# Kernel tuning notes

Hardware: AMD Instinct MI355X
Metric: run time of the kernel (lower is better)

The kernel has to match this reference:

```python
import jax, jax.numpy as jnp
import numpy as np

EPS = 1e-5
P = 2  # polynomial kernel degree


def setup_inputs() -> dict:
    key = jax.random.key(0)
    k1, k2, k3 = jax.random.split(key, 3)
    b, t, h, d = 2, 2048, 8, 64
    Q = jax.random.normal(k1, (b, t, h, d), jnp.float32)
    K = jax.random.normal(k2, (b, t, h, d), jnp.float32)
    V = jax.random.normal(k3, (b, t, h, d), jnp.float32)
    return {"Q": Q, "K": K, "V": V, "chunk_count": 16}


def reference(Q, K, V, chunk_count):
    b, t, h, d = Q.shape
    dv = V.shape[-1]
    c = chunk_count
    n = t // c  # tokens per chunk

    def to_chunked(X):
        # [b, t, h, d] -> [c, b, h, n, d]
        return X.reshape(b, c, n, h, X.shape[-1]).transpose(1, 0, 3, 2, 4)

    Qc, Kc, Vc = to_chunked(Q), to_chunked(K), to_chunked(V)

    # ---- per-chunk states: s = K^T K, S = sum_n (K_n outer K_n) outer V_n ----
    s_loc = jnp.einsum('cbhni,cbhnj->cbhij', Kc, Kc)                 # [c,b,h,d,d]
    S_loc = jnp.einsum('cbhni,cbhnj,cbhnv->cbhijv', Kc, Kc, Vc)      # [c,b,h,d,d,dv]
    # inclusive cumulative merge over chunks
    S = jnp.cumsum(S_loc, axis=0)
    s = jnp.cumsum(s_loc, axis=0)

    # ---- local within-chunk masked quadratic attention ----
    D = jnp.einsum('cbhqi,cbhki->cbhqk', Qc, Kc)                     # [c,b,h,n,n]
    C = D ** P
    mask = jnp.tril(jnp.ones((n, n), dtype=bool))
    B = jnp.where(mask, C, 0.0)
    Y = jnp.einsum('cbhqk,cbhkv->cbhqv', B, Vc)                      # [c,b,h,n,dv]
    Z = B.sum(-1) + EPS                                              # [c,b,h,n]

    # ---- cross-chunk contribution: chunk i>0 attends to state of chunks <i ----
    Qp = Qc[1:]
    Sp, sp = S[:-1], s[:-1]
    num = jnp.einsum('cbhni,cbhnj,cbhijv->cbhnv', Qp, Qp, Sp)
    den = jnp.einsum('cbhni,cbhnj,cbhij->cbhn', Qp, Qp, sp)
    Y = Y.at[1:].add(num)
    Z = Z.at[1:].add(den)

    out = (Y / Z[..., None]).transpose(1, 0, 3, 2, 4).reshape(b, t, h, dv)
    return out
```

## Files before the change

### kernel.cpp

```cpp
#include <hip/hip_runtime.h>
#include <hip/hip_fp16.h>

typedef __attribute__((ext_vector_type(8))) _Float16 f16x8;
typedef __attribute__((ext_vector_type(4))) _Float16 f16x4;
typedef __attribute__((ext_vector_type(8))) unsigned short u16x8;
typedef __attribute__((ext_vector_type(4))) float f32x4;

constexpr int NT = 256;
constexpr int TILE_SHORTS = 4096;

__device__ __forceinline__ int swzoff(int row, int c) {
    return row * 64 + ((c ^ (row & 7)) << 3);
}
__device__ __forceinline__ unsigned short f2h_u(float x) {
    return __half_as_ushort(__float2half(x));
}

__global__ __launch_bounds__(256, 4) void prepass(
    const float* __restrict__ Kg, const float* __restrict__ Vg,
    unsigned short* __restrict__ Kw, unsigned short* __restrict__ Vw)
{
    __shared__ __align__(16) float Vl[64 * 68];
    const int bid  = (int)blockIdx.x;
    const int xcd  = bid & 7;
    const int y    = bid >> 3;
    const int bh   = xcd * 2 + (y >= 32);
    const int tile = y & 31;
    const int b = bh >> 3, h = bh & 7;
    const int tid = threadIdx.x;
    const size_t gbase = (((size_t)b * 2048 + tile * 64) * 8 + h) * 64;

    #pragma unroll
    for (int j = 0; j < 4; ++j) {
        int id = j * 256 + tid, row = id >> 4, c4 = id & 15;
        *(float4*)&Vl[row * 68 + c4 * 4] =
            *(const float4*)&Vg[gbase + (size_t)row * 512 + c4 * 4];
    }

    unsigned short* Ko = Kw + (size_t)(bh * 32 + tile) * TILE_SHORTS;
    #pragma unroll
    for (int j = 0; j < 2; ++j) {
        int id = j * 256 + tid, row = id >> 3, c = id & 7;
        const float* src = &Kg[gbase + (size_t)row * 512 + c * 8];
        float4 x = *(const float4*)src, y2 = *(const float4*)(src + 4);
        u16x8 o;
        o[0] = f2h_u(x.x); o[1] = f2h_u(x.y); o[2] = f2h_u(x.z); o[3] = f2h_u(x.w);
        o[4] = f2h_u(y2.x); o[5] = f2h_u(y2.y); o[6] = f2h_u(y2.z); o[7] = f2h_u(y2.w);
        *(u16x8*)&Ko[swzoff(row, c)] = o;
    }
    __syncthreads();

    unsigned short* Vo = Vw + (size_t)(bh * 32 + tile) * TILE_SHORTS;
    #pragma unroll
    for (int j = 0; j < 2; ++j) {
        int id = j * 256 + tid, vrow = id >> 3, g = id & 7;
        u16x8 o;
        #pragma unroll
        for (int jj = 0; jj < 8; ++jj) {
            int kk = ((g & 1) * 2 + (jj >> 2)) * 16 + (g >> 1) * 4 + (jj & 3);
            o[jj] = f2h_u(Vl[kk * 68 + vrow]);
        }
        *(u16x8*)&Vo[swzoff(vrow, g)] = o;
    }
}

__global__ __launch_bounds__(NT, 3) void attn_pow2_f16(
    const float* __restrict__ Qg,
    const unsigned short* __restrict__ Kw, const unsigned short* __restrict__ Vw,
    float* __restrict__ Og)
{
    __shared__ __align__(16) unsigned short lds[4 * TILE_SHORTS];
    unsigned short* const Kb = lds;
    unsigned short* const Vb = lds + 2 * TILE_SHORTS;
    const int tid  = threadIdx.x;
    const int lane = tid & 63;
    const int wave = tid >> 6;
    const int a    = lane & 15;
    const int quad = lane >> 4;
    const int m0   = wave * 16;

    const int bid = (int)blockIdx.x;
    const int xcd = bid & 7;
    const int y   = bid >> 3;
    const int yy  = y & 31;
    const int bh  = xcd * 2 + (y >= 32);
    const int qt  = (y < 32) ? (31 - yy) : yy;
    const int b = bh >> 3, h = bh & 7;
    const int q0 = qt * 64;

    f16x8 bQ[2];
    {
        const size_t qrowbase = (((size_t)b * 2048 + q0 + m0 + a) * 8 + h) * 64;
        #pragma unroll
        for (int ks = 0; ks < 2; ++ks) {
            const float* src = &Qg[qrowbase + ks * 32 + quad * 8];
            float4 x = *(const float4*)src, y2 = *(const float4*)(src + 4);
            u16x8 o;
            o[0] = f2h_u(x.x); o[1] = f2h_u(x.y); o[2] = f2h_u(x.z); o[3] = f2h_u(x.w);
            o[4] = f2h_u(y2.x); o[5] = f2h_u(y2.y); o[6] = f2h_u(y2.z); o[7] = f2h_u(y2.w);
            bQ[ks] = __builtin_bit_cast(f16x8, o);
        }
    }

    const unsigned short* Ktiles = Kw + (size_t)bh * 32 * TILE_SHORTS;
    const unsigned short* Vtiles = Vw + (size_t)bh * 32 * TILE_SHORTS;

    u16x8 rKA[2], rVA[2], rKB[2], rVB[2];
    auto gloadA = [&](int kt) {
        const u16x8* kg = (const u16x8*)(Ktiles + (size_t)kt * TILE_SHORTS);
        const u16x8* vg = (const u16x8*)(Vtiles + (size_t)kt * TILE_SHORTS);
        rKA[0] = kg[tid * 2]; rKA[1] = kg[tid * 2 + 1];
        rVA[0] = vg[tid * 2]; rVA[1] = vg[tid * 2 + 1];
    };
    auto gloadB = [&](int kt) {
        const u16x8* kg = (const u16x8*)(Ktiles + (size_t)kt * TILE_SHORTS);
        const u16x8* vg = (const u16x8*)(Vtiles + (size_t)kt * TILE_SHORTS);
        rKB[0] = kg[tid * 2]; rKB[1] = kg[tid * 2 + 1];
        rVB[0] = vg[tid * 2]; rVB[1] = vg[tid * 2 + 1];
    };

    f32x4 oacc[4];
    #pragma unroll
    for (int n = 0; n < 4; ++n) oacc[n] = (f32x4){0.f, 0.f, 0.f, 0.f};
    float den_l = 0.f;

    union U8 { u16x8 u; f16x4 q[2]; f16x8 f; };

    auto compute = [&](const unsigned short* Kc, const unsigned short* Vc,
                       bool diag) {
        f32x4 sacc[4];
        #pragma unroll
        for (int s = 0; s < 4; ++s) sacc[s] = (f32x4){0.f, 0.f, 0.f, 0.f};
        #pragma unroll
        for (int s = 0; s < 4; ++s) {
            #pragma unroll
            for (int ks = 0; ks < 2; ++ks) {
                U8 ak; ak.u = *(const u16x8*)&Kc[swzoff(s * 16 + a, ks * 4 + quad)];
                sacc[s] = __builtin_amdgcn_mfma_f32_16x16x32_f16(ak.f, bQ[ks], sacc[s], 0, 0, 0);
            }
        }

        f16x4 aS[4];
        #pragma unroll
        for (int s = 0; s < 4; ++s) {
            float p[4];
            #pragma unroll
            for (int r = 0; r < 4; ++r) {
                float d0 = sacc[s][r];
                float v = d0 * d0;
                if (diag && (s * 16 + quad * 4 + r) > (m0 + a)) v = 0.f;
                p[r] = v;
            }
            den_l += (p[0] + p[1]) + (p[2] + p[3]);
            aS[s] = (f16x4){(_Float16)p[0], (_Float16)p[1], (_Float16)p[2], (_Float16)p[3]};
        }

        #pragma unroll
        for (int n = 0; n < 4; ++n) {
            U8 va, vb;
            va.u = *(const u16x8*)&Vc[swzoff(n * 16 + a, quad * 2)];
            vb.u = *(const u16x8*)&Vc[swzoff(n * 16 + a, quad * 2 + 1)];
            oacc[n] = __builtin_amdgcn_mfma_f32_16x16x16f16(aS[0], va.q[0], oacc[n], 0, 0, 0);
            oacc[n] = __builtin_amdgcn_mfma_f32_16x16x16f16(aS[1], va.q[1], oacc[n], 0, 0, 0);
            oacc[n] = __builtin_amdgcn_mfma_f32_16x16x16f16(aS[2], vb.q[0], oacc[n], 0, 0, 0);
            oacc[n] = __builtin_amdgcn_mfma_f32_16x16x16f16(aS[3], vb.q[1], oacc[n], 0, 0, 0);
        }
    };

    gloadA(0);
    if (qt >= 1) gloadB(1);

    int kt = 0;
    for (;;) {
        {
            u16x8* kd = (u16x8*)Kb;
            u16x8* vd = (u16x8*)Vb;
            kd[tid * 2] = rKA[0]; kd[tid * 2 + 1] = rKA[1];
            vd[tid * 2] = rVA[0]; vd[tid * 2 + 1] = rVA[1];
        }
        __syncthreads();
        if (kt + 2 <= qt) gloadA(kt + 2);
        compute(Kb, Vb, kt == qt);
        if (++kt > qt) break;

        {
            u16x8* kd = (u16x8*)(Kb + TILE_SHORTS);
            u16x8* vd = (u16x8*)(Vb + TILE_SHORTS);
            kd[tid * 2] = rKB[0]; kd[tid * 2 + 1] = rKB[1];
            vd[tid * 2] = rVB[0]; vd[tid * 2 + 1] = rVB[1];
        }
        __syncthreads();
        if (kt + 2 <= qt) gloadB(kt + 2);
        compute(Kb + TILE_SHORTS, Vb + TILE_SHORTS, kt == qt);
        if (++kt > qt) break;
    }

    den_l += __shfl_xor(den_l, 16);
    den_l += __shfl_xor(den_l, 32);

    float invz[4];
    #pragma unroll
    for (int r = 0; r < 4; ++r) {
        float dq = __shfl(den_l, quad * 4 + r);
        invz[r] = 1.0f / (dq + 1e-5f);
    }

    #pragma unroll
    for (int n = 0; n < 4; ++n) {
        #pragma unroll
        for (int r = 0; r < 4; ++r) {
            int t = q0 + m0 + quad * 4 + r;
            int v = n * 16 + a;
            Og[(((size_t)b * 2048 + t) * 8 + h) * 64 + v] = oacc[n][r] * invz[r];
        }
    }
}

extern "C" void kernel_launch(void* const* d_in, const int* in_sizes, int n_in,
                              void* d_out, int out_size, void* d_ws, size_t ws_size,
                              hipStream_t stream) {
    const float* Q = (const float*)d_in[0];
    const float* K = (const float*)d_in[1];
    const float* V = (const float*)d_in[2];
    float* O = (float*)d_out;
    unsigned short* Kw = (unsigned short*)d_ws;
    unsigned short* Vw = Kw + (size_t)16 * 32 * TILE_SHORTS;

    prepass<<<dim3(512), 256, 0, stream>>>(K, V, Kw, Vw);
    attn_pow2_f16<<<dim3(512), NT, 0, stream>>>(Q, Kw, Vw, O);
}
```

Baseline: 99.76 us.

## Load K/V fragments straight from global into registers, dropping LDS staging

The attention kernel no longer stages K/V tiles through shared memory with block barriers. Each lane now loads its own MFMA operand fragments directly from the pre-swizzled global workspace into a double-buffered register set, and s_setprio is raised around the MFMA sections. This removes the LDS writes, LDS reads and __syncthreads per tile. The cost is that every wave fetches the full tile from global/L2, four times the global traffic per block, and register pressure rises enough that launch bounds drop from 3 to 2 blocks per CU.

```diff
diff --git a/kernel.cpp b/kernel.cpp
--- a/kernel.cpp
+++ b/kernel.cpp
@@ -64,14 +64,11 @@
     }
 }
 
-__global__ __launch_bounds__(NT, 3) void attn_pow2_f16(
+__global__ __launch_bounds__(NT, 2) void attn_pow2_f16(
     const float* __restrict__ Qg,
     const unsigned short* __restrict__ Kw, const unsigned short* __restrict__ Vw,
     float* __restrict__ Og)
 {
-    __shared__ __align__(16) unsigned short lds[4 * TILE_SHORTS];
-    unsigned short* const Kb = lds;
-    unsigned short* const Vb = lds + 2 * TILE_SHORTS;
     const int tid  = threadIdx.x;
     const int lane = tid & 63;
     const int wave = tid >> 6;
@@ -105,19 +102,29 @@
     const unsigned short* Ktiles = Kw + (size_t)bh * 32 * TILE_SHORTS;
     const unsigned short* Vtiles = Vw + (size_t)bh * 32 * TILE_SHORTS;
 
-    u16x8 rKA[2], rVA[2], rKB[2], rVB[2];
-    auto gloadA = [&](int kt) {
-        const u16x8* kg = (const u16x8*)(Ktiles + (size_t)kt * TILE_SHORTS);
-        const u16x8* vg = (const u16x8*)(Vtiles + (size_t)kt * TILE_SHORTS);
-        rKA[0] = kg[tid * 2]; rKA[1] = kg[tid * 2 + 1];
-        rVA[0] = vg[tid * 2]; rVA[1] = vg[tid * 2 + 1];
-    };
-    auto gloadB = [&](int kt) {
-        const u16x8* kg = (const u16x8*)(Ktiles + (size_t)kt * TILE_SHORTS);
-        const u16x8* vg = (const u16x8*)(Vtiles + (size_t)kt * TILE_SHORTS);
-        rKB[0] = kg[tid * 2]; rKB[1] = kg[tid * 2 + 1];
-        rVB[0] = vg[tid * 2]; rVB[1] = vg[tid * 2 + 1];
-    };
+    int offK[8];
+    #pragma unroll
+    for (int s = 0; s < 4; ++s)
+        #pragma unroll
+        for (int ks = 0; ks < 2; ++ks)
+            offK[s * 2 + ks] = swzoff(s * 16 + a, ks * 4 + quad);
+    int offV[8];
+    #pragma unroll
+    for (int n = 0; n < 4; ++n)
+        #pragma unroll
+        for (int h2 = 0; h2 < 2; ++h2)
+            offV[n * 2 + h2] = swzoff(n * 16 + a, quad * 2 + h2);
+
+    u16x8 kA[8], vA[8], kB[8], vB[8];
+
+#define LOADSTAGE(kr, vr, ktile) do {                                          \
+        const unsigned short* Kt_ = Ktiles + (size_t)(ktile) * TILE_SHORTS;    \
+        const unsigned short* Vt_ = Vtiles + (size_t)(ktile) * TILE_SHORTS;    \
+        _Pragma("unroll")                                                      \
+        for (int i_ = 0; i_ < 8; ++i_) kr[i_] = *(const u16x8*)&Kt_[offK[i_]]; \
+        _Pragma("unroll")                                                      \
+        for (int i_ = 0; i_ < 8; ++i_) vr[i_] = *(const u16x8*)&Vt_[offV[i_]]; \
+    } while (0)
 
     f32x4 oacc[4];
     #pragma unroll
@@ -126,74 +133,64 @@
 
     union U8 { u16x8 u; f16x4 q[2]; f16x8 f; };
 
-    auto compute = [&](const unsigned short* Kc, const unsigned short* Vc,
-                       bool diag) {
-        f32x4 sacc[4];
-        #pragma unroll
-        for (int s = 0; s < 4; ++s) sacc[s] = (f32x4){0.f, 0.f, 0.f, 0.f};
-        #pragma unroll
-        for (int s = 0; s < 4; ++s) {
-            #pragma unroll
-            for (int ks = 0; ks < 2; ++ks) {
-                U8 ak; ak.u = *(const u16x8*)&Kc[swzoff(s * 16 + a, ks * 4 + quad)];
-                sacc[s] = __builtin_amdgcn_mfma_f32_16x16x32_f16(ak.f, bQ[ks], sacc[s], 0, 0, 0);
-            }
-        }
-
-        f16x4 aS[4];
-        #pragma unroll
-        for (int s = 0; s < 4; ++s) {
-            float p[4];
-            #pragma unroll
-            for (int r = 0; r < 4; ++r) {
-                float d0 = sacc[s][r];
-                float v = d0 * d0;
-                if (diag && (s * 16 + quad * 4 + r) > (m0 + a)) v = 0.f;
-                p[r] = v;
-            }
-            den_l += (p[0] + p[1]) + (p[2] + p[3]);
-            aS[s] = (f16x4){(_Float16)p[0], (_Float16)p[1], (_Float16)p[2], (_Float16)p[3]};
-        }
-
-        #pragma unroll
-        for (int n = 0; n < 4; ++n) {
-            U8 va, vb;
-            va.u = *(const u16x8*)&Vc[swzoff(n * 16 + a, quad * 2)];
-            vb.u = *(const u16x8*)&Vc[swzoff(n * 16 + a, quad * 2 + 1)];
-            oacc[n] = __builtin_amdgcn_mfma_f32_16x16x16f16(aS[0], va.q[0], oacc[n], 0, 0, 0);
-            oacc[n] = __builtin_amdgcn_mfma_f32_16x16x16f16(aS[1], va.q[1], oacc[n], 0, 0, 0);
-            oacc[n] = __builtin_amdgcn_mfma_f32_16x16x16f16(aS[2], vb.q[0], oacc[n], 0, 0, 0);
-            oacc[n] = __builtin_amdgcn_mfma_f32_16x16x16f16(aS[3], vb.q[1], oacc[n], 0, 0, 0);
-        }
-    };
-
-    gloadA(0);
-    if (qt >= 1) gloadB(1);
+#define COMPUTE(kr, vr, diag) do {                                             \
+        f32x4 sacc[4];                                                         \
+        _Pragma("unroll")                                                      \
+        for (int s = 0; s < 4; ++s) sacc[s] = (f32x4){0.f, 0.f, 0.f, 0.f};     \
+        __builtin_amdgcn_s_setprio(1);                                         \
+        _Pragma("unroll")                                                      \
+        for (int s = 0; s < 4; ++s) {                                          \
+            _Pragma("unroll")                                                  \
+            for (int ks = 0; ks < 2; ++ks) {                                   \
+                U8 ak; ak.u = kr[s * 2 + ks];                                  \
+                sacc[s] = __builtin_amdgcn_mfma_f32_16x16x32_f16(              \
+                    ak.f, bQ[ks], sacc[s], 0, 0, 0);                           \
+            }                                                                  \
+        }                                                                      \
+        __builtin_amdgcn_s_setprio(0);                                         \
+        f16x4 aS[4];                                                           \
+        _Pragma("unroll")                                                      \
+        for (int s = 0; s < 4; ++s) {                                          \
+            float p0 = sacc[s][0], p1 = sacc[s][1], p2 = sacc[s][2], p3 = sacc[s][3]; \
+            p0 *= p0; p1 *= p1; p2 *= p2; p3 *= p3;                            \
+            if (diag) {                                                        \
+                int kbase = s * 16 + quad * 4, qrow = m0 + a;                  \
+                if (kbase + 0 > qrow) p0 = 0.f;                                \
+                if (kbase + 1 > qrow) p1 = 0.f;                                \
+                if (kbase + 2 > qrow) p2 = 0.f;                                \
+                if (kbase + 3 > qrow) p3 = 0.f;                                \
+            }                                                                  \
+            den_l += (p0 + p1) + (p2 + p3);                                    \
+            aS[s] = (f16x4){(_Float16)p0, (_Float16)p1, (_Float16)p2, (_Float16)p3}; \
+        }                                                                      \
+        __builtin_amdgcn_s_setprio(1);                                         \
+        _Pragma("unroll")                                                      \
+        for (int n = 0; n < 4; ++n) {                                          \
+            U8 va, vb;                                                         \
+            va.u = vr[n * 2]; vb.u = vr[n * 2 + 1];                            \
+            oacc[n] = __builtin_amdgcn_mfma_f32_16x16x16f16(aS[0], va.q[0], oacc[n], 0, 0, 0); \
+            oacc[n] = __builtin_amdgcn_mfma_f32_16x16x16f16(aS[1], va.q[1], oacc[n], 0, 0, 0); \
+            oacc[n] = __builtin_amdgcn_mfma_f32_16x16x16f16(aS[2], vb.q[0], oacc[n], 0, 0, 0); \
+            oacc[n] = __builtin_amdgcn_mfma_f32_16x16x16f16(aS[3], vb.q[1], oacc[n], 0, 0, 0); \
+        }                                                                      \
+        __builtin_amdgcn_s_setprio(0);                                         \
+    } while (0)
+
+    LOADSTAGE(kA, vA, 0);
+    if (qt >= 1) LOADSTAGE(kB, vB, 1);
 
     int kt = 0;
     for (;;) {
-        {
-            u16x8* kd = (u16x8*)Kb;
-            u16x8* vd = (u16x8*)Vb;
-            kd[tid * 2] = rKA[0]; kd[tid * 2 + 1] = rKA[1];
-            vd[tid * 2] = rVA[0]; vd[tid * 2 + 1] = rVA[1];
-        }
-        __syncthreads();
-        if (kt + 2 <= qt) gloadA(kt + 2);
-        compute(Kb, Vb, kt == qt);
+        COMPUTE(kA, vA, kt == qt);
+        if (kt + 2 <= qt) LOADSTAGE(kA, vA, kt + 2);
         if (++kt > qt) break;
-
-        {
-            u16x8* kd = (u16x8*)(Kb + TILE_SHORTS);
-            u16x8* vd = (u16x8*)(Vb + TILE_SHORTS);
-            kd[tid * 2] = rKB[0]; kd[tid * 2 + 1] = rKB[1];
-            vd[tid * 2] = rVB[0]; vd[tid * 2 + 1] = rVB[1];
-        }
-        __syncthreads();
-        if (kt + 2 <= qt) gloadB(kt + 2);
-        compute(Kb + TILE_SHORTS, Vb + TILE_SHORTS, kt == qt);
+        COMPUTE(kB, vB, kt == qt);
+        if (kt + 2 <= qt) LOADSTAGE(kB, vB, kt + 2);
         if (++kt > qt) break;
     }
+
+#undef COMPUTE
+#undef LOADSTAGE
 
     den_l += __shfl_xor(den_l, 16);
     den_l += __shfl_xor(den_l, 32);
```

Measured after the change: 104.5 us. +4.8%, slower.
